# Optimization experiments

Hardware: AMD Instinct MI355X
Metric: run time of the kernel (lower is better)

## Reference

```python
import jax, jax.numpy as jnp
import numpy as np

N = 50000   # num_nodes
T = 8       # num_time_steps
C = 64      # feature width (num_features == hidden == num_classes == 64, forced by the module's shape constraints)
E = 800000  # num_edges


def temporal_conv(x, edge_index, time_index, W, b, perturb=None):
    """Faithful TemporalAGNNConv.forward: per-timestep masked scatter-add of
    neighbor features, concat over T, linear + relu. Implemented as a single
    fused (t, dst)-bucketed segment reduce instead of T separate propagates.
    Note: self.lin is dead code in the original; self-loop addition in the
    original would crash (time_index length mismatch) so edges are used as-is.
    """
    src, dst = edge_index[0], edge_index[1]
    msgs = x[src]                                   # [E, C] gather
    seg = time_index * N + dst                      # combined (t, node) bucket
    agg = jax.ops.segment_sum(msgs, seg, num_segments=T * N)   # [T*N, C]
    cat = agg.reshape(T, N, C).transpose(1, 0, 2).reshape(N, T * C)  # [N, T*C]
    out = jax.nn.relu(cat @ W + b)                  # temporal_lin + relu
    if perturb is not None:
        out = out + perturb
    return out


def setup_inputs() -> dict:
    key = jax.random.key(0)
    ks = jax.random.split(key, 11)
    x = jax.random.normal(ks[0], (N, C), jnp.float32)
    edge_index = jax.random.randint(ks[1], (2, E), 0, N, dtype=jnp.int32)
    time_index = jax.random.randint(ks[2], (E,), 0, T, dtype=jnp.int32)
    s_t = 1.0 / np.sqrt(T * C).astype(np.float32)
    # temporal_lin weights stored as [in, out] (torch Linear transposed)
    Wt1 = jax.random.uniform(ks[3], (T * C, C), jnp.float32, -s_t, s_t)
    bt1 = jax.random.uniform(ks[4], (C,), jnp.float32, -s_t, s_t)
    Wt2 = jax.random.uniform(ks[5], (T * C, C), jnp.float32, -s_t, s_t)
    bt2 = jax.random.uniform(ks[6], (C,), jnp.float32, -s_t, s_t)
    s_a1 = 1.0 / np.sqrt(C).astype(np.float32)
    Wa1 = jax.random.uniform(ks[7], (C, 128), jnp.float32, -s_a1, s_a1)
    ba1 = jax.random.uniform(ks[8], (128,), jnp.float32, -s_a1, s_a1)
    s_a2 = 1.0 / np.sqrt(128).astype(np.float32)
    Wa2 = jax.random.uniform(ks[9], (128, C), jnp.float32, -s_a2, s_a2)
    ba2 = jax.random.uniform(ks[10], (C,), jnp.float32, -s_a2, s_a2)
    return {"x": x, "edge_index": edge_index, "time_index": time_index,
            "Wt1": Wt1, "bt1": bt1, "Wt2": Wt2, "bt2": bt2,
            "Wa1": Wa1, "ba1": ba1, "Wa2": Wa2, "ba2": ba2}


def reference(x, edge_index, time_index, Wt1, bt1, Wt2, bt2, Wa1, ba1, Wa2, ba2):
    h1 = jax.nn.relu(temporal_conv(x, edge_index, time_index, Wt1, bt1))   # conv1 + relu
    h2 = temporal_conv(h1, edge_index, time_index, Wt2, bt2)               # conv2 (output width C)
    adv = jax.nn.relu(h2 @ Wa1 + ba1) @ Wa2 + ba2                          # adversary MLP -> [N, C]
    out = temporal_conv(x, edge_index, time_index, Wt1, bt1, perturb=adv)  # conv1 again + perturbation
    return out
```

## Files before the change

### kernel.cpp

```cpp
#include <hip/hip_runtime.h>

#define N_NODES 50000
#define C_FEAT  64
#define E_EDGES 800000
#define KEYS    400000
#define NBLK1   391
#define DPB     16
#define PBLK_X  1563
#define PBLK_W  128
#define PBLK_A  64
#define PBLK_H  3128
#define DPART   6250

typedef __attribute__((ext_vector_type(8))) short short8;
typedef __attribute__((ext_vector_type(4))) float f32x4;

__device__ __forceinline__ float bf2f(unsigned short u) {
    union { unsigned int i; float f; } v; v.i = ((unsigned int)u) << 16; return v.f;
}
__device__ __forceinline__ unsigned short f2bf(float f) {
    union { float f; unsigned int i; } v; v.f = f;
    unsigned int r = v.i + 0x7fff + ((v.i >> 16) & 1);
    return (unsigned short)(r >> 16);
}

__global__ __launch_bounds__(256) void prep_hist(const float* __restrict__ x,
                                                 const float* __restrict__ W1,
                                                 const float* __restrict__ W2,
                                                 const float* __restrict__ Wa1,
                                                 const float* __restrict__ Wa2,
                                                 const int* __restrict__ dst,
                                                 const int* __restrict__ tix,
                                                 unsigned short* __restrict__ xb,
                                                 unsigned short* __restrict__ WT1,
                                                 unsigned short* __restrict__ WT2,
                                                 unsigned short* __restrict__ Wa1T,
                                                 unsigned short* __restrict__ Wa2T,
                                                 int* __restrict__ cnt) {
    const int b = blockIdx.x;
    if (b < PBLK_X) {
        int base = (b * 256 + threadIdx.x) * 8;
        if (base < N_NODES * 64) {
            float4 a = *(const float4*)(x + base);
            float4 c = *(const float4*)(x + base + 4);
            short8 o;
            o[0] = (short)f2bf(a.x); o[1] = (short)f2bf(a.y);
            o[2] = (short)f2bf(a.z); o[3] = (short)f2bf(a.w);
            o[4] = (short)f2bf(c.x); o[5] = (short)f2bf(c.y);
            o[6] = (short)f2bf(c.z); o[7] = (short)f2bf(c.w);
            *(short8*)(xb + base) = o;
        }
    } else if (b < PBLK_X + PBLK_W) {
        int i = (b - PBLK_X) * 256 + threadIdx.x;
        int n = i >> 9, k = i & 511;
        WT1[i] = f2bf(W1[k * 64 + n]);
        WT2[i] = f2bf(W2[k * 64 + n]);
    } else if (b < PBLK_X + PBLK_W + PBLK_A) {
        int i = (b - PBLK_X - PBLK_W) * 256 + threadIdx.x;
        if (i < 8192) {
            int n = i >> 6, k = i & 63;
            Wa1T[i] = f2bf(Wa1[k * 128 + n]);
        } else {
            int ii = i - 8192;
            int n = ii >> 7, k = ii & 127;
            Wa2T[ii] = f2bf(Wa2[k * 64 + n]);
        }
    } else {
        int bb = b - PBLK_X - PBLK_W - PBLK_A;
        const int g = bb & 7;
        const int lo = g * DPART;
        const int e0 = (bb >> 3) * 2048 + threadIdx.x * 8;
        if (e0 < E_EDGES) {
            int4 d0 = *(const int4*)(dst + e0);
            int4 d1 = *(const int4*)(dst + e0 + 4);
            int dd[8] = {d0.x, d0.y, d0.z, d0.w, d1.x, d1.y, d1.z, d1.w};
            #pragma unroll
            for (int k = 0; k < 8; ++k) {
                if ((unsigned)(dd[k] - lo) < (unsigned)DPART)
                    atomicAdd(&cnt[dd[k] * 8 + tix[e0 + k]], 1);
            }
        }
    }
}

__global__ __launch_bounds__(256) void scan_all(int* __restrict__ cnt,
                                                int* __restrict__ bsum,
                                                int* __restrict__ chunkoff,
                                                int* __restrict__ done) {
    __shared__ int wsum[4];
    __shared__ int ticket;
    const int tid = threadIdx.x;
    const int lane = tid & 63;
    const int wave = tid >> 6;
    const int i4 = blockIdx.x * 256 + tid;
    int4 v = make_int4(0, 0, 0, 0);
    const bool ok = (i4 * 4 < KEYS);
    if (ok) v = ((const int4*)cnt)[i4];
    int s = v.x + v.y + v.z + v.w;
    int sc = s;
    #pragma unroll
    for (int d = 1; d < 64; d <<= 1) {
        int o = __shfl_up(sc, d, 64);
        if (lane >= d) sc += o;
    }
    if (lane == 63) wsum[wave] = sc;
    __syncthreads();
    int wbase = 0;
    #pragma unroll
    for (int w = 0; w < 4; ++w) wbase += (w < wave) ? wsum[w] : 0;
    int base = wbase + sc - s;
    int4 o;
    o.x = base;
    o.y = base + v.x;
    o.z = o.y + v.y;
    o.w = o.z + v.z;
    if (ok) ((int4*)cnt)[i4] = o;
    if (tid == 255) {
        bsum[blockIdx.x] = wbase + sc;
        __threadfence();
        ticket = atomicAdd(done, 1);
    }
    __syncthreads();
    if (ticket == NBLK1 - 1 && wave == 0) {
        int carry = 0;
        #pragma unroll
        for (int g = 0; g < (NBLK1 + 63) / 64; ++g) {
            int j = g * 64 + lane;
            int val = (j < NBLK1) ? atomicAdd(&bsum[j], 0) : 0;
            int scn = val;
            #pragma unroll
            for (int d = 1; d < 64; d <<= 1) {
                int oo = __shfl_up(scn, d, 64);
                if (lane >= d) scn += oo;
            }
            if (j < NBLK1) chunkoff[j] = carry + scn - val;
            carry += __shfl(scn, 63, 64);
        }
    }
}

__global__ __launch_bounds__(256) void scatter_edges(const int* __restrict__ src,
                                                     const int* __restrict__ dst,
                                                     const int* __restrict__ tix,
                                                     int* __restrict__ cursor,
                                                     const int* __restrict__ chunkoff,
                                                     int* __restrict__ elist) {
    const int g = blockIdx.x & 7;
    const int lo = g * DPART;
    const int e0 = (blockIdx.x >> 3) * 2048 + threadIdx.x * 8;
    if (e0 < E_EDGES) {
        int4 d0 = *(const int4*)(dst + e0);
        int4 d1 = *(const int4*)(dst + e0 + 4);
        int dd[8] = {d0.x, d0.y, d0.z, d0.w, d1.x, d1.y, d1.z, d1.w};
        #pragma unroll
        for (int k = 0; k < 8; ++k) {
            if ((unsigned)(dd[k] - lo) < (unsigned)DPART) {
                int t = tix[e0 + k];
                int key = dd[k] * 8 + t;
                int pos = chunkoff[key >> 10] + atomicAdd(&cursor[key], 1);
                elist[pos] = src[e0 + k] | (t << 16);
            }
        }
    }
}

#define FLUSH(T, V)                                                                   \
    { int _t = (T);                                                                   \
      if (_t != cur) { scat[dl][cur * 64 + c] = f2bf(acc); acc = 0.f; cur = _t; }     \
      acc += (V); }

#define EDGE(K)                                                                       \
    int p##K = __builtin_amdgcn_readlane(pv, e + K);                                  \
    float v##K = bf2f(Xb[(size_t)(p##K & 0xffff) * 64 + c]);

__global__ __launch_bounds__(512, 8) void fused_conv(const unsigned short* __restrict__ Xb,
                                                     const unsigned short* __restrict__ WT,
                                                     const float* __restrict__ bias,
                                                     const int* __restrict__ segend,
                                                     const int* __restrict__ chunkoff,
                                                     const int* __restrict__ elist,
                                                     unsigned short* __restrict__ Hb) {
    __shared__ unsigned short scat[DPB][520];
    const int lane = threadIdx.x & 63;
    const int wave = threadIdx.x >> 6;
    const int dbase = blockIdx.x * DPB;
    const int c = lane;

    {
        short8 z = {};
        *(short8*)&scat[wave * 2 + 0][lane * 8] = z;
        *(short8*)&scat[wave * 2 + 1][lane * 8] = z;
    }

    int sbeg[2], send_[2], pvw[2];
    #pragma unroll
    for (int q = 0; q < 2; ++q) {
        const int d = dbase + wave * 2 + q;
        const int k0 = d * 8;
        sbeg[q]  = (d == 0) ? 0 : chunkoff[(k0 - 1) >> 10] + segend[k0 - 1];
        send_[q] = chunkoff[(k0 + 7) >> 10] + segend[k0 + 7];
    }
    #pragma unroll
    for (int q = 0; q < 2; ++q)
        pvw[q] = (lane < send_[q] - sbeg[q]) ? elist[sbeg[q] + lane] : 0;

    #pragma unroll
    for (int q = 0; q < 2; ++q) {
        const int dl = wave * 2 + q;
        int i = sbeg[q];
        const int end = send_[q];
        int pv = pvw[q];
        int cur = 0;
        float acc = 0.f;
        while (i < end) {
            int cnt = end - i; cnt = (cnt > 64) ? 64 : cnt;
            int pvn = 0;
            if (i + 64 < end) pvn = (lane < end - i - 64) ? elist[i + 64 + lane] : 0;
            int e = 0;
            for (; e + 15 < cnt; e += 16) {
                EDGE(0)  EDGE(1)  EDGE(2)  EDGE(3)
                EDGE(4)  EDGE(5)  EDGE(6)  EDGE(7)
                EDGE(8)  EDGE(9)  EDGE(10) EDGE(11)
                EDGE(12) EDGE(13) EDGE(14) EDGE(15)
                FLUSH(p0 >> 16, v0)   FLUSH(p1 >> 16, v1)
                FLUSH(p2 >> 16, v2)   FLUSH(p3 >> 16, v3)
                FLUSH(p4 >> 16, v4)   FLUSH(p5 >> 16, v5)
                FLUSH(p6 >> 16, v6)   FLUSH(p7 >> 16, v7)
                FLUSH(p8 >> 16, v8)   FLUSH(p9 >> 16, v9)
                FLUSH(p10 >> 16, v10) FLUSH(p11 >> 16, v11)
                FLUSH(p12 >> 16, v12) FLUSH(p13 >> 16, v13)
                FLUSH(p14 >> 16, v14) FLUSH(p15 >> 16, v15)
            }
            if (e + 7 < cnt) {
                EDGE(0) EDGE(1) EDGE(2) EDGE(3) EDGE(4) EDGE(5) EDGE(6) EDGE(7)
                FLUSH(p0 >> 16, v0) FLUSH(p1 >> 16, v1)
                FLUSH(p2 >> 16, v2) FLUSH(p3 >> 16, v3)
                FLUSH(p4 >> 16, v4) FLUSH(p5 >> 16, v5)
                FLUSH(p6 >> 16, v6) FLUSH(p7 >> 16, v7)
                e += 8;
            }
            if (e + 3 < cnt) {
                EDGE(0) EDGE(1) EDGE(2) EDGE(3)
                FLUSH(p0 >> 16, v0) FLUSH(p1 >> 16, v1)
                FLUSH(p2 >> 16, v2) FLUSH(p3 >> 16, v3)
                e += 4;
            }
            if (e + 1 < cnt) {
                EDGE(0) EDGE(1)
                FLUSH(p0 >> 16, v0) FLUSH(p1 >> 16, v1)
                e += 2;
            }
            if (e < cnt) {
                EDGE(0)
                FLUSH(p0 >> 16, v0)
            }
            i += 64;
            pv = pvn;
        }
        scat[dl][cur * 64 + c] = f2bf(acc);
    }
    __syncthreads();

    if (wave < 4) {
        const int m = lane & 15;
        const int quad = lane >> 4;
        const int n0 = wave * 16;
        f32x4 acc4 = {0.f, 0.f, 0.f, 0.f};
        const unsigned short* wrow = WT + (size_t)(n0 + m) * 512;
        #pragma unroll
        for (int kc = 0; kc < 16; ++kc) {
            short8 af = *(const short8*)&scat[m][kc * 32 + quad * 8];
            short8 bf = *(const short8*)(wrow + kc * 32 + quad * 8);
            acc4 = __builtin_amdgcn_mfma_f32_16x16x32_bf16(af, bf, acc4, 0, 0, 0);
        }
        const int col = n0 + m;
        const float bcol = bias[col];
        #pragma unroll
        for (int r = 0; r < 4; ++r) {
            int node = dbase + quad * 4 + r;
            Hb[(size_t)node * 64 + col] = f2bf(fmaxf(acc4[r] + bcol, 0.f));
        }
    }
}

__global__ __launch_bounds__(256) void adv_mfma(const unsigned short* __restrict__ h2b,
                                                const unsigned short* __restrict__ Wa1T,
                                                const float* __restrict__ ba1,
                                                const unsigned short* __restrict__ Wa2T,
                                                const float* __restrict__ ba2,
                                                const unsigned short* __restrict__ h1b,
                                                float* __restrict__ out) {
    __shared__ unsigned short sH[64][72];
    __shared__ unsigned short sT[64][136];
    const int nbase = blockIdx.x * 64;
    const int tid = threadIdx.x;
    const int lane = tid & 63;
    const int wave = tid >> 6;
    const int m = lane & 15;
    const int quad = lane >> 4;
    const int r0 = wave * 16;

    #pragma unroll
    for (int i = 0; i < 2; ++i) {
        int idx = tid * 2 + i;
        int row = idx >> 3;
        int c8  = (idx & 7) * 8;
        int node = nbase + row;
        short8 u = {};
        if (node < N_NODES)
            u = *(const short8*)(h2b + (size_t)node * C_FEAT + c8);
        *(short8*)&sH[row][c8] = u;
    }
    __syncthreads();

    {
        f32x4 acc1[8];
        #pragma unroll
        for (int ct = 0; ct < 8; ++ct) acc1[ct] = (f32x4){0.f, 0.f, 0.f, 0.f};
        #pragma unroll
        for (int kc = 0; kc < 2; ++kc) {
            short8 af = *(const short8*)&sH[r0 + m][kc * 32 + quad * 8];
            #pragma unroll
            for (int ct = 0; ct < 8; ++ct) {
                short8 bf = *(const short8*)(Wa1T + (size_t)(ct * 16 + m) * 64 + kc * 32 + quad * 8);
                acc1[ct] = __builtin_amdgcn_mfma_f32_16x16x32_bf16(af, bf, acc1[ct], 0, 0, 0);
            }
        }
        #pragma unroll
        for (int ct = 0; ct < 8; ++ct) {
            const int col = ct * 16 + m;
            const float b1 = ba1[col];
            #pragma unroll
            for (int r = 0; r < 4; ++r)
                sT[r0 + quad * 4 + r][col] = f2bf(fmaxf(acc1[ct][r] + b1, 0.f));
        }
    }
    __syncthreads();

    {
        f32x4 acc2[4];
        #pragma unroll
        for (int ct = 0; ct < 4; ++ct) acc2[ct] = (f32x4){0.f, 0.f, 0.f, 0.f};
        #pragma unroll
        for (int kc = 0; kc < 4; ++kc) {
            short8 af = *(const short8*)&sT[r0 + m][kc * 32 + quad * 8];
            #pragma unroll
            for (int ct = 0; ct < 4; ++ct) {
                short8 bf = *(const short8*)(Wa2T + (size_t)(ct * 16 + m) * 128 + kc * 32 + quad * 8);
                acc2[ct] = __builtin_amdgcn_mfma_f32_16x16x32_bf16(af, bf, acc2[ct], 0, 0, 0);
            }
        }
        #pragma unroll
        for (int ct = 0; ct < 4; ++ct) {
            const int col = ct * 16 + m;
            const float b2 = ba2[col];
            #pragma unroll
            for (int r = 0; r < 4; ++r) {
                int node = nbase + r0 + quad * 4 + r;
                if (node < N_NODES) {
                    float val = acc2[ct][r] + b2 + bf2f(h1b[(size_t)node * 64 + col]);
                    out[(size_t)node * 64 + col] = val;
                }
            }
        }
    }
}

extern "C" void kernel_launch(void* const* d_in, const int* in_sizes, int n_in,
                              void* d_out, int out_size, void* d_ws, size_t ws_size,
                              hipStream_t stream) {
    const float* x   = (const float*)d_in[0];
    const int*   ei  = (const int*)d_in[1];
    const int*   tix = (const int*)d_in[2];
    const float* Wt1 = (const float*)d_in[3];
    const float* bt1 = (const float*)d_in[4];
    const float* Wt2 = (const float*)d_in[5];
    const float* bt2 = (const float*)d_in[6];
    const float* Wa1 = (const float*)d_in[7];
    const float* ba1 = (const float*)d_in[8];
    const float* Wa2 = (const float*)d_in[9];
    const float* ba2 = (const float*)d_in[10];
    float* out = (float*)d_out;

    const int* src = ei;
    const int* dst = ei + E_EDGES;

    unsigned short* xb   = (unsigned short*)d_ws;
    unsigned short* h1b  = xb + (size_t)N_NODES * 64;
    unsigned short* h2b  = h1b + (size_t)N_NODES * 64;
    unsigned short* WT1  = h2b + (size_t)N_NODES * 64;
    unsigned short* WT2  = WT1 + 64 * 512;
    unsigned short* Wa1T = WT2 + 64 * 512;
    unsigned short* Wa2T = Wa1T + 8192;
    int* cnt      = (int*)(Wa2T + 8192);
    int* bsum     = cnt + KEYS;
    int* chunkoff = bsum + 512;
    int* done     = chunkoff + 512;
    int* elist    = done + 64;

    const int cBlk = N_NODES / DPB;
    const int aBlk = (N_NODES + 63) / 64;

    hipMemsetAsync(cnt, 0, (KEYS + 512 + 512 + 64) * sizeof(int), stream);
    prep_hist<<<PBLK_X + PBLK_W + PBLK_A + PBLK_H, 256, 0, stream>>>(
        x, Wt1, Wt2, Wa1, Wa2, dst, tix, xb, WT1, WT2, Wa1T, Wa2T, cnt);
    scan_all<<<NBLK1, 256, 0, stream>>>(cnt, bsum, chunkoff, done);
    scatter_edges<<<8 * 391, 256, 0, stream>>>(src, dst, tix, cnt, chunkoff, elist);

    fused_conv<<<cBlk, 512, 0, stream>>>(xb,  WT1, bt1, cnt, chunkoff, elist, h1b);
    fused_conv<<<cBlk, 512, 0, stream>>>(h1b, WT2, bt2, cnt, chunkoff, elist, h2b);

    adv_mfma<<<aBlk, 256, 0, stream>>>(h2b, Wa1T, ba1, Wa2T, ba2, h1b, out);
}
```

Measured before the change: 288.4 us.

## Use one wave per destination node in fused_conv and vectorize edge loads

The fused_conv kernel now launches 1024 threads per block, so each of the 16 waves handles a single destination node instead of each of 8 waves handling two nodes in sequence. This raises the parallelism available for hiding gather latency. The cost is larger blocks, more register pressure under launch_bounds(1024,8), and possibly lower occupancy. The histogram and scatter kernels also load tix and src as int4 vectors instead of doing per-edge scalar loads.

```diff
diff --git a/kernel.cpp b/kernel.cpp
--- a/kernel.cpp
+++ b/kernel.cpp
@@ -73,11 +73,14 @@
         if (e0 < E_EDGES) {
             int4 d0 = *(const int4*)(dst + e0);
             int4 d1 = *(const int4*)(dst + e0 + 4);
+            int4 t0 = *(const int4*)(tix + e0);
+            int4 t1 = *(const int4*)(tix + e0 + 4);
             int dd[8] = {d0.x, d0.y, d0.z, d0.w, d1.x, d1.y, d1.z, d1.w};
+            int tt[8] = {t0.x, t0.y, t0.z, t0.w, t1.x, t1.y, t1.z, t1.w};
             #pragma unroll
             for (int k = 0; k < 8; ++k) {
                 if ((unsigned)(dd[k] - lo) < (unsigned)DPART)
-                    atomicAdd(&cnt[dd[k] * 8 + tix[e0 + k]], 1);
+                    atomicAdd(&cnt[dd[k] * 8 + tt[k]], 1);
             }
         }
     }
@@ -151,14 +154,19 @@
     if (e0 < E_EDGES) {
         int4 d0 = *(const int4*)(dst + e0);
         int4 d1 = *(const int4*)(dst + e0 + 4);
+        int4 t0 = *(const int4*)(tix + e0);
+        int4 t1 = *(const int4*)(tix + e0 + 4);
+        int4 s0 = *(const int4*)(src + e0);
+        int4 s1 = *(const int4*)(src + e0 + 4);
         int dd[8] = {d0.x, d0.y, d0.z, d0.w, d1.x, d1.y, d1.z, d1.w};
+        int tt[8] = {t0.x, t0.y, t0.z, t0.w, t1.x, t1.y, t1.z, t1.w};
+        int ss[8] = {s0.x, s0.y, s0.z, s0.w, s1.x, s1.y, s1.z, s1.w};
         #pragma unroll
         for (int k = 0; k < 8; ++k) {
             if ((unsigned)(dd[k] - lo) < (unsigned)DPART) {
-                int t = tix[e0 + k];
-                int key = dd[k] * 8 + t;
+                int key = dd[k] * 8 + tt[k];
                 int pos = chunkoff[key >> 10] + atomicAdd(&cursor[key], 1);
-                elist[pos] = src[e0 + k] | (t << 16);
+                elist[pos] = ss[k] | (tt[k] << 16);
             }
         }
     }
@@ -173,49 +181,39 @@
     int p##K = __builtin_amdgcn_readlane(pv, e + K);                                  \
     float v##K = bf2f(Xb[(size_t)(p##K & 0xffff) * 64 + c]);
 
-__global__ __launch_bounds__(512, 8) void fused_conv(const unsigned short* __restrict__ Xb,
-                                                     const unsigned short* __restrict__ WT,
-                                                     const float* __restrict__ bias,
-                                                     const int* __restrict__ segend,
-                                                     const int* __restrict__ chunkoff,
-                                                     const int* __restrict__ elist,
-                                                     unsigned short* __restrict__ Hb) {
+__global__ __launch_bounds__(1024, 8) void fused_conv(const unsigned short* __restrict__ Xb,
+                                                      const unsigned short* __restrict__ WT,
+                                                      const float* __restrict__ bias,
+                                                      const int* __restrict__ segend,
+                                                      const int* __restrict__ chunkoff,
+                                                      const int* __restrict__ elist,
+                                                      unsigned short* __restrict__ Hb) {
     __shared__ unsigned short scat[DPB][520];
     const int lane = threadIdx.x & 63;
     const int wave = threadIdx.x >> 6;
     const int dbase = blockIdx.x * DPB;
     const int c = lane;
+    const int dl = wave;
 
     {
         short8 z = {};
-        *(short8*)&scat[wave * 2 + 0][lane * 8] = z;
-        *(short8*)&scat[wave * 2 + 1][lane * 8] = z;
-    }
-
-    int sbeg[2], send_[2], pvw[2];
-    #pragma unroll
-    for (int q = 0; q < 2; ++q) {
-        const int d = dbase + wave * 2 + q;
-        const int k0 = d * 8;
-        sbeg[q]  = (d == 0) ? 0 : chunkoff[(k0 - 1) >> 10] + segend[k0 - 1];
-        send_[q] = chunkoff[(k0 + 7) >> 10] + segend[k0 + 7];
-    }
-    #pragma unroll
-    for (int q = 0; q < 2; ++q)
-        pvw[q] = (lane < send_[q] - sbeg[q]) ? elist[sbeg[q] + lane] : 0;
-
-    #pragma unroll
-    for (int q = 0; q < 2; ++q) {
-        const int dl = wave * 2 + q;
-        int i = sbeg[q];
-        const int end = send_[q];
-        int pv = pvw[q];
+        *(short8*)&scat[wave][lane * 8] = z;
+    }
+
+    const int d = dbase + wave;
+    const int k0 = d * 8;
+    const int sbeg = (d == 0) ? 0 : chunkoff[(k0 - 1) >> 10] + segend[k0 - 1];
+    const int send = chunkoff[(k0 + 7) >> 10] + segend[k0 + 7];
+    int pv = (lane < send - sbeg) ? elist[sbeg + lane] : 0;
+
+    {
+        int i = sbeg;
         int cur = 0;
         float acc = 0.f;
-        while (i < end) {
-            int cnt = end - i; cnt = (cnt > 64) ? 64 : cnt;
+        while (i < send) {
+            int cnt = send - i; cnt = (cnt > 64) ? 64 : cnt;
             int pvn = 0;
-            if (i + 64 < end) pvn = (lane < end - i - 64) ? elist[i + 64 + lane] : 0;
+            if (i + 64 < send) pvn = (lane < send - i - 64) ? elist[i + 64 + lane] : 0;
             int e = 0;
             for (; e + 15 < cnt; e += 16) {
                 EDGE(0)  EDGE(1)  EDGE(2)  EDGE(3)
@@ -407,8 +405,8 @@
     scan_all<<<NBLK1, 256, 0, stream>>>(cnt, bsum, chunkoff, done);
     scatter_edges<<<8 * 391, 256, 0, stream>>>(src, dst, tix, cnt, chunkoff, elist);
 
-    fused_conv<<<cBlk, 512, 0, stream>>>(xb,  WT1, bt1, cnt, chunkoff, elist, h1b);
-    fused_conv<<<cBlk, 512, 0, stream>>>(h1b, WT2, bt2, cnt, chunkoff, elist, h2b);
+    fused_conv<<<cBlk, 1024, 0, stream>>>(xb,  WT1, bt1, cnt, chunkoff, elist, h1b);
+    fused_conv<<<cBlk, 1024, 0, stream>>>(h1b, WT2, bt2, cnt, chunkoff, elist, h2b);
 
     adv_mfma<<<aBlk, 256, 0, stream>>>(h2b, Wa1T, ba1, Wa2T, ba2, h1b, out);
 }
```

New measurement: 296.2 us. +2.7%, slower.

## Drop dst-partitioned edge passes and make fused_conv a persistent grid-stride kernel

Applied to the files above, without the earlier changes.

The histogram and scatter kernels no longer split edges into 8 destination-range partitions that each reread the full edge arrays. Each edge is now processed once, with vectorised loads of dst, tix and src. fused_conv becomes a persistent kernel over 1024 blocks that loops over node tiles, with an extra barrier per tile. This removes the redundant edge reads, but the old partitioning may have existed to keep atomics local in L2, so atomic contention and scattered writes may rise.

```diff
diff --git a/kernel.cpp b/kernel.cpp
--- a/kernel.cpp
+++ b/kernel.cpp
@@ -6,11 +6,12 @@
 #define KEYS    400000
 #define NBLK1   391
 #define DPB     16
+#define NTILES  (N_NODES / DPB)
 #define PBLK_X  1563
 #define PBLK_W  128
 #define PBLK_A  64
-#define PBLK_H  3128
-#define DPART   6250
+#define PBLK_H  391
+#define CONV_GRID 1024
 
 typedef __attribute__((ext_vector_type(8))) short short8;
 typedef __attribute__((ext_vector_type(4))) float f32x4;
@@ -67,18 +68,17 @@
         }
     } else {
         int bb = b - PBLK_X - PBLK_W - PBLK_A;
-        const int g = bb & 7;
-        const int lo = g * DPART;
-        const int e0 = (bb >> 3) * 2048 + threadIdx.x * 8;
+        const int e0 = bb * 2048 + threadIdx.x * 8;
         if (e0 < E_EDGES) {
             int4 d0 = *(const int4*)(dst + e0);
             int4 d1 = *(const int4*)(dst + e0 + 4);
+            int4 t0 = *(const int4*)(tix + e0);
+            int4 t1 = *(const int4*)(tix + e0 + 4);
             int dd[8] = {d0.x, d0.y, d0.z, d0.w, d1.x, d1.y, d1.z, d1.w};
-            #pragma unroll
-            for (int k = 0; k < 8; ++k) {
-                if ((unsigned)(dd[k] - lo) < (unsigned)DPART)
-                    atomicAdd(&cnt[dd[k] * 8 + tix[e0 + k]], 1);
-            }
+            int tt[8] = {t0.x, t0.y, t0.z, t0.w, t1.x, t1.y, t1.z, t1.w};
+            #pragma unroll
+            for (int k = 0; k < 8; ++k)
+                atomicAdd(&cnt[dd[k] * 8 + tt[k]], 1);
         }
     }
 }
@@ -145,21 +145,22 @@
                                                      int* __restrict__ cursor,
                                                      const int* __restrict__ chunkoff,
                                                      int* __restrict__ elist) {
-    const int g = blockIdx.x & 7;
-    const int lo = g * DPART;
-    const int e0 = (blockIdx.x >> 3) * 2048 + threadIdx.x * 8;
+    const int e0 = blockIdx.x * 2048 + threadIdx.x * 8;
     if (e0 < E_EDGES) {
         int4 d0 = *(const int4*)(dst + e0);
         int4 d1 = *(const int4*)(dst + e0 + 4);
+        int4 t0 = *(const int4*)(tix + e0);
+        int4 t1 = *(const int4*)(tix + e0 + 4);
+        int4 s0 = *(const int4*)(src + e0);
+        int4 s1 = *(const int4*)(src + e0 + 4);
         int dd[8] = {d0.x, d0.y, d0.z, d0.w, d1.x, d1.y, d1.z, d1.w};
+        int tt[8] = {t0.x, t0.y, t0.z, t0.w, t1.x, t1.y, t1.z, t1.w};
+        int ss[8] = {s0.x, s0.y, s0.z, s0.w, s1.x, s1.y, s1.z, s1.w};
         #pragma unroll
         for (int k = 0; k < 8; ++k) {
-            if ((unsigned)(dd[k] - lo) < (unsigned)DPART) {
-                int t = tix[e0 + k];
-                int key = dd[k] * 8 + t;
-                int pos = chunkoff[key >> 10] + atomicAdd(&cursor[key], 1);
-                elist[pos] = src[e0 + k] | (t << 16);
-            }
+            int key = dd[k] * 8 + tt[k];
+            int pos = chunkoff[key >> 10] + atomicAdd(&cursor[key], 1);
+            elist[pos] = ss[k] | (tt[k] << 16);
         }
     }
 }
@@ -183,103 +184,107 @@
     __shared__ unsigned short scat[DPB][520];
     const int lane = threadIdx.x & 63;
     const int wave = threadIdx.x >> 6;
-    const int dbase = blockIdx.x * DPB;
     const int c = lane;
 
-    {
-        short8 z = {};
-        *(short8*)&scat[wave * 2 + 0][lane * 8] = z;
-        *(short8*)&scat[wave * 2 + 1][lane * 8] = z;
-    }
-
-    int sbeg[2], send_[2], pvw[2];
-    #pragma unroll
-    for (int q = 0; q < 2; ++q) {
-        const int d = dbase + wave * 2 + q;
-        const int k0 = d * 8;
-        sbeg[q]  = (d == 0) ? 0 : chunkoff[(k0 - 1) >> 10] + segend[k0 - 1];
-        send_[q] = chunkoff[(k0 + 7) >> 10] + segend[k0 + 7];
-    }
-    #pragma unroll
-    for (int q = 0; q < 2; ++q)
-        pvw[q] = (lane < send_[q] - sbeg[q]) ? elist[sbeg[q] + lane] : 0;
-
-    #pragma unroll
-    for (int q = 0; q < 2; ++q) {
-        const int dl = wave * 2 + q;
-        int i = sbeg[q];
-        const int end = send_[q];
-        int pv = pvw[q];
-        int cur = 0;
-        float acc = 0.f;
-        while (i < end) {
-            int cnt = end - i; cnt = (cnt > 64) ? 64 : cnt;
-            int pvn = 0;
-            if (i + 64 < end) pvn = (lane < end - i - 64) ? elist[i + 64 + lane] : 0;
-            int e = 0;
-            for (; e + 15 < cnt; e += 16) {
-                EDGE(0)  EDGE(1)  EDGE(2)  EDGE(3)
-                EDGE(4)  EDGE(5)  EDGE(6)  EDGE(7)
-                EDGE(8)  EDGE(9)  EDGE(10) EDGE(11)
-                EDGE(12) EDGE(13) EDGE(14) EDGE(15)
-                FLUSH(p0 >> 16, v0)   FLUSH(p1 >> 16, v1)
-                FLUSH(p2 >> 16, v2)   FLUSH(p3 >> 16, v3)
-                FLUSH(p4 >> 16, v4)   FLUSH(p5 >> 16, v5)
-                FLUSH(p6 >> 16, v6)   FLUSH(p7 >> 16, v7)
-                FLUSH(p8 >> 16, v8)   FLUSH(p9 >> 16, v9)
-                FLUSH(p10 >> 16, v10) FLUSH(p11 >> 16, v11)
-                FLUSH(p12 >> 16, v12) FLUSH(p13 >> 16, v13)
-                FLUSH(p14 >> 16, v14) FLUSH(p15 >> 16, v15)
-            }
-            if (e + 7 < cnt) {
-                EDGE(0) EDGE(1) EDGE(2) EDGE(3) EDGE(4) EDGE(5) EDGE(6) EDGE(7)
-                FLUSH(p0 >> 16, v0) FLUSH(p1 >> 16, v1)
-                FLUSH(p2 >> 16, v2) FLUSH(p3 >> 16, v3)
-                FLUSH(p4 >> 16, v4) FLUSH(p5 >> 16, v5)
-                FLUSH(p6 >> 16, v6) FLUSH(p7 >> 16, v7)
-                e += 8;
-            }
-            if (e + 3 < cnt) {
-                EDGE(0) EDGE(1) EDGE(2) EDGE(3)
-                FLUSH(p0 >> 16, v0) FLUSH(p1 >> 16, v1)
-                FLUSH(p2 >> 16, v2) FLUSH(p3 >> 16, v3)
-                e += 4;
-            }
-            if (e + 1 < cnt) {
-                EDGE(0) EDGE(1)
-                FLUSH(p0 >> 16, v0) FLUSH(p1 >> 16, v1)
-                e += 2;
-            }
-            if (e < cnt) {
-                EDGE(0)
-                FLUSH(p0 >> 16, v0)
-            }
-            i += 64;
-            pv = pvn;
-        }
-        scat[dl][cur * 64 + c] = f2bf(acc);
-    }
-    __syncthreads();
-
-    if (wave < 4) {
-        const int m = lane & 15;
-        const int quad = lane >> 4;
-        const int n0 = wave * 16;
-        f32x4 acc4 = {0.f, 0.f, 0.f, 0.f};
-        const unsigned short* wrow = WT + (size_t)(n0 + m) * 512;
-        #pragma unroll
-        for (int kc = 0; kc < 16; ++kc) {
-            short8 af = *(const short8*)&scat[m][kc * 32 + quad * 8];
-            short8 bf = *(const short8*)(wrow + kc * 32 + quad * 8);
-            acc4 = __builtin_amdgcn_mfma_f32_16x16x32_bf16(af, bf, acc4, 0, 0, 0);
-        }
-        const int col = n0 + m;
-        const float bcol = bias[col];
-        #pragma unroll
-        for (int r = 0; r < 4; ++r) {
-            int node = dbase + quad * 4 + r;
-            Hb[(size_t)node * 64 + col] = f2bf(fmaxf(acc4[r] + bcol, 0.f));
-        }
+    for (int tile = blockIdx.x; tile < NTILES; tile += gridDim.x) {
+        const int dbase = tile * DPB;
+
+        {
+            short8 z = {};
+            *(short8*)&scat[wave * 2 + 0][lane * 8] = z;
+            *(short8*)&scat[wave * 2 + 1][lane * 8] = z;
+        }
+
+        int sbeg[2], send_[2], pvw[2];
+        #pragma unroll
+        for (int q = 0; q < 2; ++q) {
+            const int d = dbase + wave * 2 + q;
+            const int k0 = d * 8;
+            sbeg[q]  = (d == 0) ? 0 : chunkoff[(k0 - 1) >> 10] + segend[k0 - 1];
+            send_[q] = chunkoff[(k0 + 7) >> 10] + segend[k0 + 7];
+        }
+        #pragma unroll
+        for (int q = 0; q < 2; ++q)
+            pvw[q] = (lane < send_[q] - sbeg[q]) ? elist[sbeg[q] + lane] : 0;
+
+        #pragma unroll
+        for (int q = 0; q < 2; ++q) {
+            const int dl = wave * 2 + q;
+            int i = sbeg[q];
+            const int end = send_[q];
+            int pv = pvw[q];
+            int cur = 0;
+            float acc = 0.f;
+            while (i < end) {
+                int cnt = end - i; cnt = (cnt > 64) ? 64 : cnt;
+                int pvn = 0;
+                if (i + 64 < end) pvn = (lane < end - i - 64) ? elist[i + 64 + lane] : 0;
+                int e = 0;
+                for (; e + 15 < cnt; e += 16) {
+                    EDGE(0)  EDGE(1)  EDGE(2)  EDGE(3)
+                    EDGE(4)  EDGE(5)  EDGE(6)  EDGE(7)
+                    EDGE(8)  EDGE(9)  EDGE(10) EDGE(11)
+                    EDGE(12) EDGE(13) EDGE(14) EDGE(15)
+                    FLUSH(p0 >> 16, v0)   FLUSH(p1 >> 16, v1)
+                    FLUSH(p2 >> 16, v2)   FLUSH(p3 >> 16, v3)
+                    FLUSH(p4 >> 16, v4)   FLUSH(p5 >> 16, v5)
+                    FLUSH(p6 >> 16, v6)   FLUSH(p7 >> 16, v7)
+                    FLUSH(p8 >> 16, v8)   FLUSH(p9 >> 16, v9)
+                    FLUSH(p10 >> 16, v10) FLUSH(p11 >> 16, v11)
+                    FLUSH(p12 >> 16, v12) FLUSH(p13 >> 16, v13)
+                    FLUSH(p14 >> 16, v14) FLUSH(p15 >> 16, v15)
+                }
+                if (e + 7 < cnt) {
+                    EDGE(0) EDGE(1) EDGE(2) EDGE(3) EDGE(4) EDGE(5) EDGE(6) EDGE(7)
+                    FLUSH(p0 >> 16, v0) FLUSH(p1 >> 16, v1)
+                    FLUSH(p2 >> 16, v2) FLUSH(p3 >> 16, v3)
+                    FLUSH(p4 >> 16, v4) FLUSH(p5 >> 16, v5)
+                    FLUSH(p6 >> 16, v6) FLUSH(p7 >> 16, v7)
+                    e += 8;
+                }
+                if (e + 3 < cnt) {
+                    EDGE(0) EDGE(1) EDGE(2) EDGE(3)
+                    FLUSH(p0 >> 16, v0) FLUSH(p1 >> 16, v1)
+                    FLUSH(p2 >> 16, v2) FLUSH(p3 >> 16, v3)
+                    e += 4;
+                }
+                if (e + 1 < cnt) {
+                    EDGE(0) EDGE(1)
+                    FLUSH(p0 >> 16, v0) FLUSH(p1 >> 16, v1)
+                    e += 2;
+                }
+                if (e < cnt) {
+                    EDGE(0)
+                    FLUSH(p0 >> 16, v0)
+                }
+                i += 64;
+                pv = pvn;
+            }
+            scat[dl][cur * 64 + c] = f2bf(acc);
+        }
+        __syncthreads();
+
+        if (wave < 4) {
+            const int m = lane & 15;
+            const int quad = lane >> 4;
+            const int n0 = wave * 16;
+            f32x4 acc4 = {0.f, 0.f, 0.f, 0.f};
+            const unsigned short* wrow = WT + (size_t)(n0 + m) * 512;
+            #pragma unroll
+            for (int kc = 0; kc < 16; ++kc) {
+                short8 af = *(const short8*)&scat[m][kc * 32 + quad * 8];
+                short8 bf = *(const short8*)(wrow + kc * 32 + quad * 8);
+                acc4 = __builtin_amdgcn_mfma_f32_16x16x32_bf16(af, bf, acc4, 0, 0, 0);
+            }
+            const int col = n0 + m;
+            const float bcol = bias[col];
+            #pragma unroll
+            for (int r = 0; r < 4; ++r) {
+                int node = dbase + quad * 4 + r;
+                Hb[(size_t)node * 64 + col] = f2bf(fmaxf(acc4[r] + bcol, 0.f));
+            }
+        }
+        __syncthreads();
     }
 }
 
@@ -398,17 +403,16 @@
     int* done     = chunkoff + 512;
     int* elist    = done + 64;
 
-    const int cBlk = N_NODES / DPB;
     const int aBlk = (N_NODES + 63) / 64;
 
     hipMemsetAsync(cnt, 0, (KEYS + 512 + 512 + 64) * sizeof(int), stream);
     prep_hist<<<PBLK_X + PBLK_W + PBLK_A + PBLK_H, 256, 0, stream>>>(
         x, Wt1, Wt2, Wa1, Wa2, dst, tix, xb, WT1, WT2, Wa1T, Wa2T, cnt);
     scan_all<<<NBLK1, 256, 0, stream>>>(cnt, bsum, chunkoff, done);
-    scatter_edges<<<8 * 391, 256, 0, stream>>>(src, dst, tix, cnt, chunkoff, elist);
-
-    fused_conv<<<cBlk, 512, 0, stream>>>(xb,  WT1, bt1, cnt, chunkoff, elist, h1b);
-    fused_conv<<<cBlk, 512, 0, stream>>>(h1b, WT2, bt2, cnt, chunkoff, elist, h2b);
+    scatter_edges<<<391, 256, 0, stream>>>(src, dst, tix, cnt, chunkoff, elist);
+
+    fused_conv<<<CONV_GRID, 512, 0, stream>>>(xb,  WT1, bt1, cnt, chunkoff, elist, h1b);
+    fused_conv<<<CONV_GRID, 512, 0, stream>>>(h1b, WT2, bt2, cnt, chunkoff, elist, h2b);
 
     adv_mfma<<<aBlk, 256, 0, stream>>>(h2b, Wa1T, ba1, Wa2T, ba2, h1b, out);
 }
```

After: 294.7 us. 1.02x slower.
